# Performance work log

Hardware: AMD Instinct MI355X
Metric: run time of the kernel (lower is better)

## Reference

```python
import jax, jax.numpy as jnp
import numpy as np

S, B, D = 1024, 2, 1024      # seq, batch, embed_dim
E, TOPK = 15, 3              # routed experts = 8*2-1, top_n = 2*2-1
F = 1024                     # per-expert ffn dim (ffn_dim // m)
FS = 2048                    # shared expert ffn dim (ffn_dim * n_shared)


def _uinit(k, shape, out_dim):
    std = out_dim ** -0.5
    return jax.random.uniform(k, shape, jnp.float32, -std, std)


def setup_inputs() -> dict:
    key = jax.random.key(0)
    ks = jax.random.split(key, 10)
    return {
        "x": jax.random.normal(ks[0], (S, B, D), jnp.float32),
        "gate_w": jax.random.normal(ks[1], (E, D), jnp.float32) * (D ** -0.5),
        "fc1_w": _uinit(ks[2], (E, 2 * F, D), 2 * F),
        "fc1_b": _uinit(ks[3], (E, 2 * F), 2 * F),
        "geglu_mult": jnp.ones((E, F), jnp.float32),
        "fc2_w": _uinit(ks[4], (E, D, F), D),
        "fc2_b": _uinit(ks[5], (E, D), D),
        "s_fc1_w": _uinit(ks[6], (2 * FS, D), 2 * FS),
        "s_fc1_b": _uinit(ks[7], (2 * FS,), 2 * FS),
        "s_geglu_mult": jnp.ones((FS,), jnp.float32),
        "s_fc2_w": _uinit(ks[8], (D, FS), D),
        "s_fc2_b": _uinit(ks[9], (D,), D),
    }


def reference(x, gate_w, fc1_w, fc1_b, geglu_mult, fc2_w, fc2_b,
              s_fc1_w, s_fc1_b, s_geglu_mult, s_fc2_w, s_fc2_b):
    s, b, d = x.shape
    xt = x.reshape(-1, d)                              # [T, D] tokens
    T = xt.shape[0]

    # --- gate: softmax over routed experts, top-k, renormalize ---
    logits = xt @ gate_w.T                             # [T, E]
    scores = jax.nn.softmax(logits, axis=-1)
    topk_w, topk_idx = jax.lax.top_k(scores, TOPK)     # [T, K]
    topk_w = topk_w / (jnp.sum(topk_w, axis=-1, keepdims=True) + 1e-20)
    # combine weights: zero for non-routed experts (same math as dispatch/scatter)
    comb = jnp.zeros((T, E), xt.dtype).at[jnp.arange(T)[:, None], topk_idx].add(topk_w)

    # --- routed experts: GEGLU FFN applied as grouped GEMM, weighted combine ---
    h = jnp.einsum('td,efd->etf', xt, fc1_w) + fc1_b[:, None, :]   # [E, T, 2F]
    xh, g = h[..., :F], h[..., F:]                                 # chunk: (x, gate)
    a = jax.nn.gelu(g, approximate=False) * xh * geglu_mult[:, None, :]
    yexp = jnp.einsum('etf,edf->etd', a, fc2_w) + fc2_b[:, None, :]  # [E, T, D]
    y = jnp.einsum('etd,te->td', yexp, comb)                         # [T, D]

    # --- shared expert ---
    hs = xt @ s_fc1_w.T + s_fc1_b                      # [T, 2*FS]
    xs, gs = hs[..., :FS], hs[..., FS:]
    as_ = jax.nn.gelu(gs, approximate=False) * xs * s_geglu_mult
    ys = as_ @ s_fc2_w.T + s_fc2_b                     # [T, D]

    return (y + ys).reshape(s, b, d)
```

## Files before the change

kernel.cpp:

```cpp
#include <hip/hip_runtime.h>

typedef __attribute__((ext_vector_type(8))) short bfrag;
typedef __attribute__((ext_vector_type(4))) float f32x4;

__device__ __forceinline__ short f2bf(float f) {
  union { float f; unsigned u; } v; v.f = f;
  unsigned r = v.u + 0x7FFFu + ((v.u >> 16) & 1u);
  return (short)(r >> 16);
}
__device__ __forceinline__ float bf2f(unsigned short h) {
  union { unsigned u; float f; } v; v.u = ((unsigned)h) << 16;
  return v.f;
}
__device__ __forceinline__ float gelu_exact(float g) {
  return 0.5f * g * (1.0f + erff(g * 0.70710678118654752f));
}
__device__ __forceinline__ void gld_lds16(const short* g, short* l) {
  __builtin_amdgcn_global_load_lds(
      (const __attribute__((address_space(1))) void*)g,
      (__attribute__((address_space(3))) void*)l, 16, 0, 0);
}

__global__ __launch_bounds__(256) void k_convert_w(
    const float* __restrict__ s0, const float* __restrict__ s1,
    const float* __restrict__ s2, const float* __restrict__ s3,
    short* __restrict__ d0, short* __restrict__ d1,
    short* __restrict__ d2, short* __restrict__ d3)
{
  const int b = blockIdx.x;
  const float* s; short* d; long off;
  if (b < 3840)      { s = s0; d = d0; off = (long)b * 2048; }
  else if (b < 5760) { s = s1; d = d1; off = (long)(b - 3840) * 2048; }
  else if (b < 6272) { s = s2; d = d2; off = (long)(b - 5760) * 2048; }
  else               { s = s3; d = d3; off = (long)(b - 6272) * 2048; }
  const f32x4* sp = (const f32x4*)s;
  const long i0 = off + threadIdx.x;
  f32x4 v[8];
#pragma unroll
  for (int j = 0; j < 8; j++) v[j] = __builtin_nontemporal_load(sp + i0 + j * 256);
#pragma unroll
  for (int j = 0; j < 8; j++)
    ((short4*)d)[i0 + j * 256] =
        make_short4(f2bf(v[j].x), f2bf(v[j].y), f2bf(v[j].z), f2bf(v[j].w));
}

__global__ __launch_bounds__(64) void k_gate(const float* __restrict__ x,
    const float* __restrict__ gw, int* __restrict__ topk_idx,
    float* __restrict__ topk_w, short* __restrict__ xbf)
{
  const int t0 = blockIdx.x * 4;
  const int lane = threadIdx.x;
  float xv[4][16];
#pragma unroll
  for (int tt = 0; tt < 4; tt++)
#pragma unroll
    for (int i = 0; i < 16; i++) {
      xv[tt][i] = x[(size_t)(t0 + tt) * 1024 + lane + 64 * i];
      xbf[(size_t)(t0 + tt) * 1024 + lane + 64 * i] = f2bf(xv[tt][i]);
    }
  float p[4][15];
#pragma unroll
  for (int e = 0; e < 15; e++) {
    float wv[16];
#pragma unroll
    for (int i = 0; i < 16; i++) wv[i] = gw[(size_t)e * 1024 + lane + 64 * i];
#pragma unroll
    for (int tt = 0; tt < 4; tt++) {
      float s = 0.f;
#pragma unroll
      for (int i = 0; i < 16; i++) s += xv[tt][i] * wv[i];
#pragma unroll
      for (int o = 32; o; o >>= 1) s += __shfl_xor(s, o, 64);
      p[tt][e] = s;
    }
  }
#pragma unroll
  for (int tt = 0; tt < 4; tt++) {
    float m = -1e30f;
#pragma unroll
    for (int e = 0; e < 15; e++) m = fmaxf(m, p[tt][e]);
    float q[15], Z = 0.f;
#pragma unroll
    for (int e = 0; e < 15; e++) { q[e] = expf(p[tt][e] - m); Z += q[e]; }
    int usedMask = 0; int bi[3]; float bv[3];
#pragma unroll
    for (int j = 0; j < 3; j++) {
      float best = -1.f; int b = 0;
#pragma unroll
      for (int e = 0; e < 15; e++) {
        bool ok = (!((usedMask >> e) & 1)) && (q[e] > best);
        if (ok) { best = q[e]; b = e; }
      }
      bi[j] = b; bv[j] = best / Z; usedMask |= 1 << b;
    }
    if (lane == tt) {
      float den = bv[0] + bv[1] + bv[2] + 1e-20f;
#pragma unroll
      for (int j = 0; j < 3; j++) {
        topk_idx[(t0 + tt) * 3 + j] = bi[j];
        topk_w[(t0 + tt) * 3 + j] = bv[j] / den;
      }
    }
  }
}

__global__ __launch_bounds__(1024) void k_route(const int* __restrict__ topk_idx,
    const float* __restrict__ topk_w, int* __restrict__ cnt_g, int* __restrict__ offs_g,
    int* __restrict__ row_tok, float* __restrict__ row_wt, int* __restrict__ row_id)
{
  __shared__ int scnt[16], soffs[16], sfill[16];
  const int tid = threadIdx.x;
  if (tid < 16) { scnt[tid] = 0; sfill[tid] = 0; }
  __syncthreads();
  for (int i = tid; i < 6144; i += 1024) atomicAdd(&scnt[topk_idx[i]], 1);
  __syncthreads();
  if (tid == 0) {
    int a = 0;
    for (int e = 0; e < 15; e++) { soffs[e] = a; offs_g[e] = a; cnt_g[e] = scnt[e]; a += scnt[e]; }
  }
  __syncthreads();
  for (int i = tid; i < 6144; i += 1024) {
    int e = topk_idx[i];
    int pos = atomicAdd(&sfill[e], 1);
    int row = soffs[e] + pos;
    row_tok[row] = i / 3;
    row_wt[row] = topk_w[i];
    row_id[i] = row;
  }
}

__device__ __forceinline__ bool resolve_tile128(const int* __restrict__ cnt, int ty,
                                                int& e, int& lt) {
  int acc = 0;
#pragma unroll
  for (int i = 0; i < 15; i++) {
    int tl = (cnt[i] + 127) >> 7;
    if (ty < acc + tl) { e = i; lt = ty - acc; return true; }
    acc += tl;
  }
  return false;
}

__global__ __launch_bounds__(256) void k_fc1(
    const short* __restrict__ xbf,
    const short* __restrict__ wsh, const float* __restrict__ bsh, const float* __restrict__ msh,
    const short* __restrict__ wex, const float* __restrict__ bex, const float* __restrict__ mex,
    const int* __restrict__ cnt, const int* __restrict__ offs, const int* __restrict__ row_tok,
    short* __restrict__ as_buf, short* __restrict__ a_buf)
{
  __shared__ short smem[4 * 128 * 64];
  const int tid = threadIdx.x;
  const int bid = blockIdx.x;
  const bool sh = bid < 512;
  int f0, m0 = 0, e = 0, rowBase = 0, nrows = 128;
  if (sh) {
    f0 = (bid & 31) * 64; m0 = (bid >> 5) * 128;
  } else {
    const int b2 = bid - 512;
    int lt;
    if (!resolve_tile128(cnt, b2 >> 4, e, lt)) return;
    f0 = (b2 & 15) * 64;
    rowBase = offs[e] + lt * 128;
    nrows = cnt[e] - lt * 128; if (nrows > 128) nrows = 128;
  }
  const int lane = tid & 63, ml = lane & 15, kq = lane >> 4, mlo = lane & 7;
  const int wv = tid >> 6, wr = wv >> 1, wc = wv & 1;
  const int lrow = lane >> 3, lchk = lane & 7;
  const int Fhalf = sh ? 2048 : 1024;
  const short* wptr = sh ? wsh : (wex + (size_t)e * 2048 * 1024);
  const short* aSrc[4]; const short* bSrc[4];
#pragma unroll
  for (int t = 0; t < 4; t++) {
    const int r = wv * 32 + t * 8 + lrow;
    const int sc = (lchk ^ (r & 7)) * 8;
    if (sh) aSrc[t] = xbf + (size_t)(m0 + r) * 1024 + sc;
    else {
      const int rc = r < nrows ? r : nrows - 1;
      aSrc[t] = xbf + (size_t)row_tok[rowBase + rc] * 1024 + sc;
    }
    const int grow = (r < 64) ? (f0 + r) : (Fhalf + f0 + r - 64);
    bSrc[t] = wptr + (size_t)grow * 1024 + sc;
  }
  f32x4 acc[4][4] = {};

#define FC1_STAGE(BUF, K0) do {                                              \
    short* A_ = smem + (BUF) * 16384;                                        \
    short* B_ = A_ + 8192;                                                   \
    _Pragma("unroll")                                                        \
    for (int t = 0; t < 4; t++) gld_lds16(aSrc[t] + (K0), A_ + (wv * 32 + t * 8) * 64); \
    _Pragma("unroll")                                                        \
    for (int t = 0; t < 4; t++) gld_lds16(bSrc[t] + (K0), B_ + (wv * 32 + t * 8) * 64); \
  } while (0)

#define FC1_COMPUTE(BUF) do {                                                \
    const short* As_ = smem + (BUF) * 16384;                                 \
    const short* Bs_ = As_ + 8192;                                           \
    _Pragma("unroll")                                                        \
    for (int kk = 0; kk < 2; kk++) {                                         \
      const int so = ((kk * 4 + kq) ^ mlo) * 8;                              \
      bfrag af[4], bb[4];                                                    \
      _Pragma("unroll")                                                      \
      for (int i = 0; i < 4; i++)                                            \
        af[i] = *(const bfrag*)&As_[(wr * 64 + i * 16 + ml) * 64 + so];      \
      _Pragma("unroll")                                                      \
      for (int j = 0; j < 4; j++) {                                          \
        const int brow = ((j >> 1) ? 64 : 0) + wc * 32 + (j & 1) * 16 + ml;  \
        bb[j] = *(const bfrag*)&Bs_[brow * 64 + so];                         \
      }                                                                      \
      _Pragma("unroll")                                                      \
      for (int i = 0; i < 4; i++)                                            \
        _Pragma("unroll")                                                    \
        for (int j = 0; j < 4; j++)                                          \
          acc[i][j] = __builtin_amdgcn_mfma_f32_16x16x32_bf16(af[i], bb[j], acc[i][j], 0, 0, 0); \
    }                                                                        \
  } while (0)

  FC1_STAGE(0, 0);
  __syncthreads();
  int cur = 0;
  for (int ks = 0; ks < 15; ks++) {
    FC1_STAGE(cur ^ 1, (ks + 1) * 64);
    FC1_COMPUTE(cur);
    __syncthreads();
    cur ^= 1;
  }
  FC1_COMPUTE(cur);

  const float* bias = sh ? bsh : (bex + (size_t)e * 2048);
  const float* mult = sh ? msh : (mex + (size_t)e * 1024);
#pragma unroll
  for (int jj = 0; jj < 2; jj++) {
    const int fl = wc * 32 + jj * 16 + ml;
    const int f = f0 + fl;
    const float b1 = bias[f];
    const float b2 = bias[Fhalf + f];
    const float mv = mult[f];
#pragma unroll
    for (int i = 0; i < 4; i++)
#pragma unroll
      for (int rg = 0; rg < 4; rg++) {
        const int row = wr * 64 + i * 16 + kq * 4 + rg;
        const float h1 = acc[i][jj][rg] + b1;
        const float h2 = acc[i][jj + 2][rg] + b2;
        const short o = f2bf(gelu_exact(h2) * h1 * mv);
        if (sh) as_buf[(size_t)(m0 + row) * 2048 + f] = o;
        else if (row < nrows) a_buf[(size_t)(rowBase + row) * 1024 + f] = o;
      }
  }
}

__global__ __launch_bounds__(256) void k_fc2(
    const short* __restrict__ as_buf, const short* __restrict__ wsfc2, const float* __restrict__ s_b,
    const short* __restrict__ a_buf, const short* __restrict__ wfc2, const float* __restrict__ e_b,
    const int* __restrict__ cnt, const int* __restrict__ offs, const float* __restrict__ row_wt,
    float* __restrict__ y, short* __restrict__ yexp)
{
  __shared__ short smem[4 * 128 * 64];
  const int tid = threadIdx.x;
  const int bid = blockIdx.x;
  const bool sh = bid < 128;
  int d0, m0 = 0, e = 0, rowBase = 0, nrows = 128, Klen, astr, bstr;
  const short *aBase, *bBase;
  if (sh) {
    d0 = (bid & 7) * 128; m0 = (bid >> 3) * 128;
    Klen = 2048; astr = 2048; bstr = 2048;
    aBase = as_buf; bBase = wsfc2;
  } else {
    const int b2 = bid - 128;
    int lt;
    if (!resolve_tile128(cnt, b2 >> 3, e, lt)) return;
    d0 = (b2 & 7) * 128;
    rowBase = offs[e] + lt * 128;
    nrows = cnt[e] - lt * 128; if (nrows > 128) nrows = 128;
    Klen = 1024; astr = 1024; bstr = 1024;
    aBase = a_buf + (size_t)rowBase * 1024;
    bBase = wfc2 + (size_t)e * 1024 * 1024;
  }
  const int lane = tid & 63, ml = lane & 15, kq = lane >> 4, mlo = lane & 7;
  const int wv = tid >> 6, wr = wv >> 1, wc = wv & 1;
  const int lrow = lane >> 3, lchk = lane & 7;
  const short* aSrc[4]; const short* bSrc[4];
#pragma unroll
  for (int t = 0; t < 4; t++) {
    const int r = wv * 32 + t * 8 + lrow;
    const int sc = (lchk ^ (r & 7)) * 8;
    aSrc[t] = aBase + (size_t)(sh ? (m0 + r) : r) * astr + sc;
    bSrc[t] = bBase + (size_t)(d0 + r) * bstr + sc;
  }
  f32x4 acc[4][4] = {};

#define FC2_STAGE(BUF, K0) do {                                              \
    short* A_ = smem + (BUF) * 16384;                                        \
    short* B_ = A_ + 8192;                                                   \
    _Pragma("unroll")                                                        \
    for (int t = 0; t < 4; t++) gld_lds16(aSrc[t] + (K0), A_ + (wv * 32 + t * 8) * 64); \
    _Pragma("unroll")                                                        \
    for (int t = 0; t < 4; t++) gld_lds16(bSrc[t] + (K0), B_ + (wv * 32 + t * 8) * 64); \
  } while (0)

#define FC2_COMPUTE(BUF) do {                                                \
    const short* As_ = smem + (BUF) * 16384;                                 \
    const short* Bs_ = As_ + 8192;                                           \
    _Pragma("unroll")                                                        \
    for (int kk = 0; kk < 2; kk++) {                                         \
      const int so = ((kk * 4 + kq) ^ mlo) * 8;                              \
      bfrag af[4], bb[4];                                                    \
      _Pragma("unroll")                                                      \
      for (int i = 0; i < 4; i++)                                            \
        af[i] = *(const bfrag*)&As_[(wr * 64 + i * 16 + ml) * 64 + so];      \
      _Pragma("unroll")                                                      \
      for (int j = 0; j < 4; j++)                                            \
        bb[j] = *(const bfrag*)&Bs_[(wc * 64 + j * 16 + ml) * 64 + so];      \
      _Pragma("unroll")                                                      \
      for (int i = 0; i < 4; i++)                                            \
        _Pragma("unroll")                                                    \
        for (int j = 0; j < 4; j++)                                          \
          acc[i][j] = __builtin_amdgcn_mfma_f32_16x16x32_bf16(af[i], bb[j], acc[i][j], 0, 0, 0); \
    }                                                                        \
  } while (0)

  FC2_STAGE(0, 0);
  __syncthreads();
  int cur = 0;
  const int NK = Klen >> 6;
  for (int ks = 0; ks < NK - 1; ks++) {
    FC2_STAGE(cur ^ 1, (ks + 1) * 64);
    FC2_COMPUTE(cur);
    __syncthreads();
    cur ^= 1;
  }
  FC2_COMPUTE(cur);

#pragma unroll
  for (int j = 0; j < 4; j++) {
    const int d = d0 + wc * 64 + j * 16 + ml;
    const float bv = sh ? s_b[d] : e_b[(size_t)e * 1024 + d];
#pragma unroll
    for (int i = 0; i < 4; i++)
#pragma unroll
      for (int rg = 0; rg < 4; rg++) {
        const int row = wr * 64 + i * 16 + kq * 4 + rg;
        if (sh) {
          y[(size_t)(m0 + row) * 1024 + d] = acc[i][j][rg] + bv;
        } else if (row < nrows) {
          const float wt = row_wt[rowBase + row];
          yexp[(size_t)(rowBase + row) * 1024 + d] = f2bf((acc[i][j][rg] + bv) * wt);
        }
      }
  }
}

__global__ __launch_bounds__(256) void k_combine(float* __restrict__ y,
    const short* __restrict__ yexp, const int* __restrict__ row_id)
{
  const int idx = blockIdx.x * 256 + threadIdx.x;
  const int t = idx >> 8;
  const int d4 = (idx & 255) * 4;
  const int r0 = row_id[t * 3], r1 = row_id[t * 3 + 1], r2 = row_id[t * 3 + 2];
  float4 acc = *(float4*)(y + (size_t)t * 1024 + d4);
  const ushort4 v0 = *(const ushort4*)(yexp + (size_t)r0 * 1024 + d4);
  const ushort4 v1 = *(const ushort4*)(yexp + (size_t)r1 * 1024 + d4);
  const ushort4 v2 = *(const ushort4*)(yexp + (size_t)r2 * 1024 + d4);
  acc.x += bf2f(v0.x) + bf2f(v1.x) + bf2f(v2.x);
  acc.y += bf2f(v0.y) + bf2f(v1.y) + bf2f(v2.y);
  acc.z += bf2f(v0.z) + bf2f(v1.z) + bf2f(v2.z);
  acc.w += bf2f(v0.w) + bf2f(v1.w) + bf2f(v2.w);
  *(float4*)(y + (size_t)t * 1024 + d4) = acc;
}

extern "C" void kernel_launch(void* const* d_in, const int* in_sizes, int n_in,
                              void* d_out, int out_size, void* d_ws, size_t ws_size,
                              hipStream_t stream) {
  const float* x          = (const float*)d_in[0];
  const float* gate_w     = (const float*)d_in[1];
  const float* fc1_w      = (const float*)d_in[2];
  const float* fc1_b      = (const float*)d_in[3];
  const float* geglu_mult = (const float*)d_in[4];
  const float* fc2_w      = (const float*)d_in[5];
  const float* fc2_b      = (const float*)d_in[6];
  const float* s_fc1_w    = (const float*)d_in[7];
  const float* s_fc1_b    = (const float*)d_in[8];
  const float* s_mult     = (const float*)d_in[9];
  const float* s_fc2_w    = (const float*)d_in[10];
  const float* s_fc2_b    = (const float*)d_in[11];
  float* y = (float*)d_out;

  char* wsb = (char*)d_ws;
  int*   cnt      = (int*)(wsb + 0);
  int*   offs     = (int*)(wsb + 64);
  int*   topk_idx = (int*)(wsb + 256);
  float* topk_w   = (float*)(wsb + 24832);
  int*   row_tok  = (int*)(wsb + 49408);
  float* row_wt   = (float*)(wsb + 74496);
  int*   row_id   = (int*)(wsb + 99584);
  short* xbf      = (short*)(wsb + 131072);
  short* a_buf    = (short*)(wsb + 8519680);
  short* as_buf   = (short*)(wsb + 21364736);
  short* yexp     = (short*)(wsb + 29753344);
  short* wbf_sfc1 = (short*)(wsb + 42598400);
  short* wbf_sfc2 = (short*)(wsb + 50987008);
  short* wbf_fc1  = (short*)(wsb + 55181312);
  short* wbf_fc2  = (short*)(wsb + 118095872);

  k_convert_w<<<6528, 256, 0, stream>>>(fc1_w, fc2_w, s_fc1_w, s_fc2_w,
                                        wbf_fc1, wbf_fc2, wbf_sfc1, wbf_sfc2);
  k_gate<<<512, 64, 0, stream>>>(x, gate_w, topk_idx, topk_w, xbf);
  k_route<<<1, 1024, 0, stream>>>(topk_idx, topk_w, cnt, offs, row_tok, row_wt, row_id);
  k_fc1<<<1520, 256, 0, stream>>>(xbf, wbf_sfc1, s_fc1_b, s_mult,
                                  wbf_fc1, fc1_b, geglu_mult,
                                  cnt, offs, row_tok, as_buf, a_buf);
  k_fc2<<<632, 256, 0, stream>>>(as_buf, wbf_sfc2, s_fc2_b,
                                 a_buf, wbf_fc2, fc2_b,
                                 cnt, offs, row_wt, y, yexp);
  k_combine<<<2048, 256, 0, stream>>>(y, yexp, row_id);
}
```

Measured before the change: 430.3 us.

## Deepen FC1/FC2 GEMM pipelines to four LDS stages with vmcnt waits

Replaces the double-buffered K loop in both the fc1 and fc2 grouped GEMM kernels with a four-stage LDS ring that keeps three tiles in flight. Each iteration waits on a partial vmcnt instead of a full __syncthreads, so global-to-LDS loads can overlap more compute. The aim is to hide memory latency better. LDS per block doubles (128 KB), which may lower occupancy. The hand-tuned vmcnt counts must match the number of load instructions each stage issues.

New measurement: 451.8 us. 5.0% more time.

```diff
diff --git a/kernel.cpp b/kernel.cpp
--- a/kernel.cpp
+++ b/kernel.cpp
@@ -148,7 +148,7 @@
     const int* __restrict__ cnt, const int* __restrict__ offs, const int* __restrict__ row_tok,
     short* __restrict__ as_buf, short* __restrict__ a_buf)
 {
-  __shared__ short smem[4 * 128 * 64];
+  __shared__ short smem[4 * 16384];
   const int tid = threadIdx.x;
   const int bid = blockIdx.x;
   const bool sh = bid < 512;
@@ -216,15 +216,18 @@
   } while (0)
 
   FC1_STAGE(0, 0);
-  __syncthreads();
-  int cur = 0;
-  for (int ks = 0; ks < 15; ks++) {
-    FC1_STAGE(cur ^ 1, (ks + 1) * 64);
-    FC1_COMPUTE(cur);
-    __syncthreads();
-    cur ^= 1;
-  }
-  FC1_COMPUTE(cur);
+  FC1_STAGE(1, 64);
+  FC1_STAGE(2, 128);
+#pragma unroll 4
+  for (int ks = 0; ks < 16; ks++) {
+    if (ks < 14)       asm volatile("s_waitcnt vmcnt(16)" ::: "memory");
+    else if (ks == 14) asm volatile("s_waitcnt vmcnt(8)" ::: "memory");
+    else               asm volatile("s_waitcnt vmcnt(0)" ::: "memory");
+    __builtin_amdgcn_s_barrier();
+    __builtin_amdgcn_sched_barrier(0);
+    if (ks + 3 < 16) FC1_STAGE((ks + 3) & 3, (ks + 3) * 64);
+    FC1_COMPUTE(ks & 3);
+  }
 
   const float* bias = sh ? bsh : (bex + (size_t)e * 2048);
   const float* mult = sh ? msh : (mex + (size_t)e * 1024);
@@ -255,7 +258,7 @@
     const int* __restrict__ cnt, const int* __restrict__ offs, const float* __restrict__ row_wt,
     float* __restrict__ y, short* __restrict__ yexp)
 {
-  __shared__ short smem[4 * 128 * 64];
+  __shared__ short smem[4 * 16384];
   const int tid = threadIdx.x;
   const int bid = blockIdx.x;
   const bool sh = bid < 128;
@@ -320,16 +323,18 @@
   } while (0)
 
   FC2_STAGE(0, 0);
-  __syncthreads();
-  int cur = 0;
+  FC2_STAGE(1, 64);
+  FC2_STAGE(2, 128);
   const int NK = Klen >> 6;
-  for (int ks = 0; ks < NK - 1; ks++) {
-    FC2_STAGE(cur ^ 1, (ks + 1) * 64);
-    FC2_COMPUTE(cur);
-    __syncthreads();
-    cur ^= 1;
-  }
-  FC2_COMPUTE(cur);
+  for (int ks = 0; ks < NK; ks++) {
+    if (ks + 2 < NK)      asm volatile("s_waitcnt vmcnt(16)" ::: "memory");
+    else if (ks + 1 < NK) asm volatile("s_waitcnt vmcnt(8)" ::: "memory");
+    else                  asm volatile("s_waitcnt vmcnt(0)" ::: "memory");
+    __builtin_amdgcn_s_barrier();
+    __builtin_amdgcn_sched_barrier(0);
+    if (ks + 3 < NK) FC2_STAGE((ks + 3) & 3, (ks + 3) * 64);
+    FC2_COMPUTE(ks & 3);
+  }
 
 #pragma unroll
   for (int j = 0; j < 4; j++) {
```
